# Kernel tuning notes

Measured on AMD Instinct MI355X. Metric: run time of the kernel, lower is better.

## Reference

```python
import jax, jax.numpy as jnp
import numpy as np

ALPHA = 0.2  # LeakyReLU negative slope
NEG_INF = jnp.float32(-9e15)


def setup_inputs() -> dict:
    key = jax.random.key(0)
    k1, k2, k3, k4, k5, k6 = jax.random.split(key, 6)
    B, N, F_in, F_out = 8, 2048, 256, 64
    h = jax.random.normal(k1, (B, N, F_in), dtype=jnp.float32)
    adj = jax.random.randint(k2, (B, N, N), 0, 2, dtype=jnp.int32)
    level = jax.random.uniform(k3, (B, N), dtype=jnp.float32)
    node_type = jax.random.uniform(k4, (B, N, N), dtype=jnp.float32)
    W = jax.random.normal(k5, (F_in, F_out), dtype=jnp.float32) * 1.414 / np.sqrt(F_in)
    a = jax.random.normal(k6, (2 * F_out, 1), dtype=jnp.float32) * 1.414 / np.sqrt(2 * F_out)
    return {"h": h, "adj": adj, "level": level, "node_type": node_type, "W": W, "a": a}


def reference(h, adj, level, node_type, W, a):
    # h: [B,N,Fin], adj/node_type: [B,N,N], level: [B,N], W: [Fin,Fout], a: [2*Fout,1]
    F_out = W.shape[1]
    Wh = jnp.einsum('bnf,fo->bno', h, W)  # [B,N,Fout]
    # Additive attention decomposed: e[b,i,j] = a1.Wh_i + a2.Wh_j (no O(N^2*2F) tensor)
    a1 = a[:F_out, 0]
    a2 = a[F_out:, 0]
    f1 = Wh @ a1  # [B,N]
    f2 = Wh @ a2  # [B,N]
    e = jax.nn.leaky_relu(f1[:, :, None] + f2[:, None, :], negative_slope=ALPHA)  # [B,N,N]
    # gat_our=True path: node_type scales scores, level scales Wh
    e = e * node_type
    Wh = Wh * level[:, :, None]
    attention = jnp.where(adj > 0, e, NEG_INF)
    attention = jax.nn.softmax(attention, axis=1)  # faithful: original softmax over dim=1
    # dropout p=0 / eval mode -> identity
    h_prime = jnp.einsum('bij,bjo->bio', attention, Wh)  # [B,N,Fout]
    return jax.nn.relu(h_prime)  # concat=True
```

## Files before the change

kernel.cpp:

```cpp
#include <hip/hip_runtime.h>

#define BB 8
#define NN 2048
#define FIN 256
#define FO 64

typedef short short8_t __attribute__((ext_vector_type(8)));
typedef float float4_t __attribute__((ext_vector_type(4)));

__device__ __forceinline__ unsigned short f2bf(float x) {
  unsigned int u = __float_as_uint(x);
  unsigned int r = (u + 0x7fffu + ((u >> 16) & 1u)) >> 16;
  return (unsigned short)r;
}

#define GLD16(gp, lp)                                                          \
  __builtin_amdgcn_global_load_lds(                                            \
      (const __attribute__((address_space(1))) void*)(gp),                     \
      (__attribute__((address_space(3))) void*)(lp), 16, 0, 0)

__global__ __launch_bounds__(256) void k1_gemm(
    const float* __restrict__ h,
    const float* __restrict__ level,
    const float* __restrict__ W,
    const float* __restrict__ a,
    float* __restrict__ V, float* __restrict__ f1, float* __restrict__ f2,
    float* __restrict__ scol)
{
  __shared__ float wlds[128 * 64];
  __shared__ float hs[16 * 260];
  __shared__ float parts1[16 * 17];
  __shared__ float parts2[16 * 17];
  int t = threadIdx.x;
  int b = blockIdx.x >> 7;
  int i0 = (blockIdx.x & 127) * 16;

  if (blockIdx.x < 64) scol[blockIdx.x * 256 + t] = 0.0f;

  {
    int r_ld = t >> 4, f0 = (t & 15) * 16;
    const float* hp = h + (size_t)(b * NN + i0 + r_ld) * FIN + f0;
    float4 x0 = *(const float4*)(hp);
    float4 x1 = *(const float4*)(hp + 4);
    float4 x2 = *(const float4*)(hp + 8);
    float4 x3 = *(const float4*)(hp + 12);
    float* hd = &hs[r_ld * 260 + f0];
    *(float4*)(hd + 0) = x0; *(float4*)(hd + 4) = x1;
    *(float4*)(hd + 8) = x2; *(float4*)(hd + 12) = x3;
  }

  int r = t >> 4;
  int c4 = (t & 15) * 4;
  float4 acc = {0, 0, 0, 0};

  #pragma unroll
  for (int half = 0; half < 2; ++half) {
    __syncthreads();
    #pragma unroll
    for (int q = 0; q < 8; ++q) {
      int idx = q * 1024 + t * 4;
      *(float4*)&wlds[idx] = *(const float4*)&W[half * 8192 + idx];
    }
    __syncthreads();
    for (int f = 0; f < 128; f += 8) {
      float4 hv0 = *(const float4*)&hs[r * 260 + half * 128 + f];
      float4 hv1 = *(const float4*)&hs[r * 260 + half * 128 + f + 4];
      float hvv[8] = {hv0.x, hv0.y, hv0.z, hv0.w, hv1.x, hv1.y, hv1.z, hv1.w};
      #pragma unroll
      for (int k = 0; k < 8; ++k) {
        float4 wv = *(const float4*)&wlds[(f + k) * 64 + c4];
        acc.x += hvv[k] * wv.x; acc.y += hvv[k] * wv.y;
        acc.z += hvv[k] * wv.z; acc.w += hvv[k] * wv.w;
      }
    }
  }

  float p1 = acc.x * a[c4] + acc.y * a[c4 + 1] + acc.z * a[c4 + 2] + acc.w * a[c4 + 3];
  float p2 = acc.x * a[64 + c4] + acc.y * a[64 + c4 + 1] +
             acc.z * a[64 + c4 + 2] + acc.w * a[64 + c4 + 3];
  parts1[r * 17 + (t & 15)] = p1;
  parts2[r * 17 + (t & 15)] = p2;
  __syncthreads();
  if (t < 16) {
    float s1 = 0.f, s2 = 0.f;
    #pragma unroll
    for (int g = 0; g < 16; ++g) { s1 += parts1[t * 17 + g]; s2 += parts2[t * 17 + g]; }
    f1[b * NN + i0 + t] = s1;
    f2[b * NN + i0 + t] = s2;
  }

  float lv = level[b * NN + i0 + r];
  float4 vv = {acc.x * lv, acc.y * lv, acc.z * lv, acc.w * lv};
  *(float4*)&V[(size_t)(b * NN + i0 + r) * FO + c4] = vv;
}

template <int STORE_U>
__global__ __launch_bounds__(512) void k2a_stats(
    const int* __restrict__ adj,
    const float* __restrict__ ntp,
    const float* __restrict__ f1,
    const float* __restrict__ f2,
    unsigned short* __restrict__ u_bf,
    unsigned char* __restrict__ bits,
    float* __restrict__ scol)
{
  __shared__ int ladj[2][16 * 256];
  __shared__ float lnt[2][16 * 256];
  __shared__ float red[2048];
  int t = threadIdx.x;
  int b = blockIdx.x >> 6;
  int row0 = (blockIdx.x & 63) * 32;
  int w = t >> 6, l = t & 63;
  size_t base = (size_t)b * NN;

  auto stage = [&](int buf, int s) {
    int tile = s >> 3, c = s & 7;
    int r0 = row0 + tile * 16 + 2 * w;
    const int* ga = adj + (base + r0) * NN + c * 256 + l * 4;
    const float* gn = ntp + (base + r0) * NN + c * 256 + l * 4;
    GLD16(ga, &ladj[buf][(2 * w) * 256]);
    GLD16(ga + NN, &ladj[buf][(2 * w + 1) * 256]);
    GLD16(gn, &lnt[buf][(2 * w) * 256]);
    GLD16(gn + NN, &lnt[buf][(2 * w + 1) * 256]);
  };

  int jj = t & 255;
  int rh = t >> 8;
  int kk_in = jj >> 5;
  int quad = (jj & 31) >> 3;
  int e = jj & 7;

  float accJ[8];
  #pragma unroll
  for (int c = 0; c < 8; ++c) accJ[c] = 0.f;
  float f2v[8];
  #pragma unroll
  for (int c = 0; c < 8; ++c) f2v[c] = f2[base + c * 256 + jj];

  stage(0, 0);
  for (int s = 0; s < 16; ++s) {
    int buf = s & 1;
    __syncthreads();
    if (s < 15) stage(buf ^ 1, s + 1);
    int tile = s >> 3, c = s & 7;
    int it = (row0 >> 4) + tile;
    size_t fbase = ((size_t)(b * 128 + it) * 64 + (c * 8 + kk_in)) * 512
                   + quad * 128 + rh * 64 + e;
    #pragma unroll
    for (int q = 0; q < 8; ++q) {
      int r = rh * 8 + q;
      int av = ladj[buf][r * 256 + jj];
      float nv = lnt[buf][r * 256 + jj];
      float f1v = f1[base + row0 + tile * 16 + r];
      float x = f1v + f2v[c];
      x = fmaxf(x, 0.2f * x);
      bool m = av > 0;
      float u = m ? __expf(x * nv) : 0.0f;
      accJ[c] += u;
      if (STORE_U) {
        u_bf[fbase + q * 8] = f2bf(u);
      } else {
        unsigned long long bal = __ballot(m);
        if (l == 0)
          *(unsigned long long*)&bits[(base + row0 + tile * 16 + r) * (NN / 8)
                                      + c * 32 + (w & 3) * 8] = bal;
      }
    }
  }

  if (rh == 0) {
    #pragma unroll
    for (int c = 0; c < 8; ++c) red[c * 256 + jj] = accJ[c];
  }
  __syncthreads();
  if (rh == 1) {
    #pragma unroll
    for (int c = 0; c < 8; ++c) red[c * 256 + jj] += accJ[c];
  }
  __syncthreads();
  #pragma unroll
  for (int q = 0; q < 4; ++q)
    atomicAdd(&scol[base + q * 512 + t], red[q * 512 + t]);
}

__global__ __launch_bounds__(256) void k2b_pack(
    const float* __restrict__ V,
    const float* __restrict__ scol,
    unsigned short* __restrict__ vf)
{
  int t = threadIdx.x;
  int b = blockIdx.x >> 6;
  int kk = blockIdx.x & 63;
  int ng = t >> 6;
  int l = t & 63;
  int jb = kk * 32 + ((l >> 4) * 8);
  int o = ng * 16 + (l & 15);
  unsigned int pk[4];
  #pragma unroll
  for (int p = 0; p < 4; ++p) {
    int jr0 = jb + 2 * p, jr1 = jb + 2 * p + 1;
    float s0 = scol[b * NN + jr0];
    float s1 = scol[b * NN + jr1];
    float i0 = (s0 > 0.f) ? (1.0f / s0) : 0.0f;
    float i1 = (s1 > 0.f) ? (1.0f / s1) : 0.0f;
    float v0 = V[(size_t)(b * NN + jr0) * FO + o] * i0;
    float v1 = V[(size_t)(b * NN + jr1) * FO + o] * i1;
    pk[p] = (unsigned int)f2bf(v0) | ((unsigned int)f2bf(v1) << 16);
  }
  *(uint4*)(vf + (size_t)(((b * 64 + kk) * 4 + ng) * 64 + l) * 8) =
      make_uint4(pk[0], pk[1], pk[2], pk[3]);
}

__global__ __launch_bounds__(256) void k3_agg_u(
    const unsigned short* __restrict__ u_bf,
    const unsigned short* __restrict__ vf,
    float* __restrict__ outp)
{
  __shared__ float red[4 * 16 * 68];
  int t = threadIdx.x;
  int b = blockIdx.x >> 7;
  int it = blockIdx.x & 127;
  int i0 = it * 16;
  int w = t >> 6, l = t & 63;
  int col = l & 15, quad = l >> 4;
  const unsigned short* abase = u_bf + ((size_t)(b * 128 + it) * 64) * 512 + l * 8;
  const unsigned short* vbase = vf + (size_t)(b * 64) * 2048 + l * 8;

  short8_t Aall[16];
  #pragma unroll
  for (int s = 0; s < 16; ++s)
    Aall[s] = *(const short8_t*)(abase + (size_t)(w * 16 + s) * 512);

  const unsigned short* vb0 = vbase + (size_t)(w * 16) * 2048;
  short8_t c0 = *(const short8_t*)(vb0);
  short8_t c1 = *(const short8_t*)(vb0 + 512);
  short8_t c2 = *(const short8_t*)(vb0 + 1024);
  short8_t c3 = *(const short8_t*)(vb0 + 1536);

  float4_t acc0 = {0, 0, 0, 0}, acc1 = {0, 0, 0, 0}, acc2 = {0, 0, 0, 0}, acc3 = {0, 0, 0, 0};

  #pragma unroll
  for (int s = 0; s < 16; ++s) {
    short8_t n0, n1, n2, n3;
    if (s < 15) {
      const unsigned short* vn = vbase + (size_t)(w * 16 + s + 1) * 2048;
      n0 = *(const short8_t*)(vn);
      n1 = *(const short8_t*)(vn + 512);
      n2 = *(const short8_t*)(vn + 1024);
      n3 = *(const short8_t*)(vn + 1536);
    }
    acc0 = __builtin_amdgcn_mfma_f32_16x16x32_bf16(Aall[s], c0, acc0, 0, 0, 0);
    acc1 = __builtin_amdgcn_mfma_f32_16x16x32_bf16(Aall[s], c1, acc1, 0, 0, 0);
    acc2 = __builtin_amdgcn_mfma_f32_16x16x32_bf16(Aall[s], c2, acc2, 0, 0, 0);
    acc3 = __builtin_amdgcn_mfma_f32_16x16x32_bf16(Aall[s], c3, acc3, 0, 0, 0);
    if (s < 15) { c0 = n0; c1 = n1; c2 = n2; c3 = n3; }
  }

  #pragma unroll
  for (int r = 0; r < 4; ++r) {
    int rowi = quad * 4 + r;
    red[w * 1088 + rowi * 68 + 0 + col] = acc0[r];
    red[w * 1088 + rowi * 68 + 16 + col] = acc1[r];
    red[w * 1088 + rowi * 68 + 32 + col] = acc2[r];
    red[w * 1088 + rowi * 68 + 48 + col] = acc3[r];
  }
  __syncthreads();

  int row = t >> 4, o4 = (t & 15) * 4;
  const float* rp = &red[row * 68 + o4];
  float4 s0 = *(const float4*)(rp);
  float4 s1 = *(const float4*)(rp + 1088);
  float4 s2 = *(const float4*)(rp + 2176);
  float4 s3 = *(const float4*)(rp + 3264);
  float4 o;
  o.x = fmaxf(s0.x + s1.x + s2.x + s3.x, 0.0f);
  o.y = fmaxf(s0.y + s1.y + s2.y + s3.y, 0.0f);
  o.z = fmaxf(s0.z + s1.z + s2.z + s3.z, 0.0f);
  o.w = fmaxf(s0.w + s1.w + s2.w + s3.w, 0.0f);
  *(float4*)&outp[(size_t)(b * NN + i0 + row) * FO + o4] = o;
}

__global__ __launch_bounds__(256) void k3_agg_b(
    const float* __restrict__ ntp,
    const unsigned char* __restrict__ bits,
    const float* __restrict__ f1,
    const float* __restrict__ f2,
    const unsigned short* __restrict__ vf,
    float* __restrict__ outp)
{
  __shared__ float red[4 * 16 * 68];
  int t = threadIdx.x;
  int b = blockIdx.x >> 7;
  int i0 = (blockIdx.x & 127) * 16;
  int w = t >> 6, l = t & 63;
  int col = l & 15, quad = l >> 4;
  int gi = b * NN + i0 + col;
  float f1v = f1[gi];
  const float* ntrow = ntp + (size_t)gi * NN;
  const unsigned char* brow = bits + (size_t)gi * (NN / 8);
  float4_t acc0 = {0, 0, 0, 0}, acc1 = {0, 0, 0, 0}, acc2 = {0, 0, 0, 0}, acc3 = {0, 0, 0, 0};

  for (int s = 0; s < 16; ++s) {
    int kk = w * 16 + s;
    int jq = kk * 32 + quad * 8;
    unsigned int m8 = brow[jq >> 3];
    float4 n0 = *(const float4*)(ntrow + jq);
    float4 n1 = *(const float4*)(ntrow + jq + 4);
    float4 g0 = *(const float4*)(f2 + b * NN + jq);
    float4 g1 = *(const float4*)(f2 + b * NN + jq + 4);
    float f2v[8] = {g0.x, g0.y, g0.z, g0.w, g1.x, g1.y, g1.z, g1.w};
    float ntf[8] = {n0.x, n0.y, n0.z, n0.w, n1.x, n1.y, n1.z, n1.w};
    union { unsigned int u[4]; short8_t v; } A;
    #pragma unroll
    for (int p = 0; p < 4; ++p) {
      int e0 = 2 * p, e1 = 2 * p + 1;
      float x0 = f1v + f2v[e0]; x0 = fmaxf(x0, 0.2f * x0);
      float u0 = ((m8 >> e0) & 1u) ? __expf(x0 * ntf[e0]) : 0.0f;
      float x1 = f1v + f2v[e1]; x1 = fmaxf(x1, 0.2f * x1);
      float u1 = ((m8 >> e1) & 1u) ? __expf(x1 * ntf[e1]) : 0.0f;
      A.u[p] = (unsigned int)f2bf(u0) | ((unsigned int)f2bf(u1) << 16);
    }
    const unsigned short* vb = vf + (size_t)(b * 64 + kk) * 2048 + l * 8;
    short8_t bf0 = *(const short8_t*)(vb);
    short8_t bf1 = *(const short8_t*)(vb + 512);
    short8_t bf2 = *(const short8_t*)(vb + 1024);
    short8_t bf3 = *(const short8_t*)(vb + 1536);
    acc0 = __builtin_amdgcn_mfma_f32_16x16x32_bf16(A.v, bf0, acc0, 0, 0, 0);
    acc1 = __builtin_amdgcn_mfma_f32_16x16x32_bf16(A.v, bf1, acc1, 0, 0, 0);
    acc2 = __builtin_amdgcn_mfma_f32_16x16x32_bf16(A.v, bf2, acc2, 0, 0, 0);
    acc3 = __builtin_amdgcn_mfma_f32_16x16x32_bf16(A.v, bf3, acc3, 0, 0, 0);
  }

  #pragma unroll
  for (int r = 0; r < 4; ++r) {
    int rowi = quad * 4 + r;
    red[w * 1088 + rowi * 68 + 0 + col] = acc0[r];
    red[w * 1088 + rowi * 68 + 16 + col] = acc1[r];
    red[w * 1088 + rowi * 68 + 32 + col] = acc2[r];
    red[w * 1088 + rowi * 68 + 48 + col] = acc3[r];
  }
  __syncthreads();

  int row = t >> 4, o4 = (t & 15) * 4;
  const float* rp = &red[row * 68 + o4];
  float4 s0 = *(const float4*)(rp);
  float4 s1 = *(const float4*)(rp + 1088);
  float4 s2 = *(const float4*)(rp + 2176);
  float4 s3 = *(const float4*)(rp + 3264);
  float4 o;
  o.x = fmaxf(s0.x + s1.x + s2.x + s3.x, 0.0f);
  o.y = fmaxf(s0.y + s1.y + s2.y + s3.y, 0.0f);
  o.z = fmaxf(s0.z + s1.z + s2.z + s3.z, 0.0f);
  o.w = fmaxf(s0.w + s1.w + s2.w + s3.w, 0.0f);
  *(float4*)&outp[(size_t)(b * NN + i0 + row) * FO + o4] = o;
}

extern "C" void kernel_launch(void* const* d_in, const int* in_sizes, int n_in,
                              void* d_out, int out_size, void* d_ws, size_t ws_size,
                              hipStream_t stream) {
  const float* h = (const float*)d_in[0];
  const int* adj = (const int*)d_in[1];
  const float* level = (const float*)d_in[2];
  const float* ntm = (const float*)d_in[3];
  const float* W = (const float*)d_in[4];
  const float* a = (const float*)d_in[5];
  float* outp = (float*)d_out;

  float* V = (float*)d_ws;
  float* f1 = V + (size_t)BB * NN * FO;
  float* f2 = f1 + BB * NN;
  float* scol = f2 + BB * NN;
  unsigned short* vf = (unsigned short*)(scol + BB * NN);
  char* tail = (char*)(vf + (size_t)BB * NN * FO);
  size_t fixed = (size_t)(tail - (char*)d_ws);
  size_t need_u = fixed + (size_t)BB * NN * NN * 2;
  bool big = (ws_size >= need_u);

  k1_gemm<<<1024, 256, 0, stream>>>(h, level, W, a, V, f1, f2, scol);
  if (big) {
    unsigned short* u_bf = (unsigned short*)tail;
    k2a_stats<1><<<512, 512, 0, stream>>>(adj, ntm, f1, f2, u_bf, nullptr, scol);
    k2b_pack<<<512, 256, 0, stream>>>(V, scol, vf);
    k3_agg_u<<<1024, 256, 0, stream>>>(u_bf, vf, outp);
  } else {
    unsigned char* bits = (unsigned char*)tail;
    k2a_stats<0><<<512, 512, 0, stream>>>(adj, ntm, f1, f2, nullptr, bits, scol);
    k2b_pack<<<512, 256, 0, stream>>>(V, scol, vf);
    k3_agg_b<<<1024, 256, 0, stream>>>(ntm, bits, f1, f2, vf, outp);
  }
}
```

Before: 346.6 us.

## Retile aggregation kernel to 64-row blocks with 8-wave K split

```diff
diff --git a/kernel.cpp b/kernel.cpp
--- a/kernel.cpp
+++ b/kernel.cpp
@@ -211,73 +211,88 @@
       make_uint4(pk[0], pk[1], pk[2], pk[3]);
 }
 
-__global__ __launch_bounds__(256) void k3_agg_u(
+__global__ __launch_bounds__(512) void k3_agg_u2(
     const unsigned short* __restrict__ u_bf,
     const unsigned short* __restrict__ vf,
     float* __restrict__ outp)
 {
-  __shared__ float red[4 * 16 * 68];
+  __shared__ float red[8 * 16 * 68];
   int t = threadIdx.x;
-  int b = blockIdx.x >> 7;
-  int it = blockIdx.x & 127;
-  int i0 = it * 16;
+  int b = blockIdx.x >> 5;
+  int tt = blockIdx.x & 31;
   int w = t >> 6, l = t & 63;
   int col = l & 15, quad = l >> 4;
-  const unsigned short* abase = u_bf + ((size_t)(b * 128 + it) * 64) * 512 + l * 8;
   const unsigned short* vbase = vf + (size_t)(b * 64) * 2048 + l * 8;
-
-  short8_t Aall[16];
-  #pragma unroll
-  for (int s = 0; s < 16; ++s)
-    Aall[s] = *(const short8_t*)(abase + (size_t)(w * 16 + s) * 512);
-
-  const unsigned short* vb0 = vbase + (size_t)(w * 16) * 2048;
-  short8_t c0 = *(const short8_t*)(vb0);
-  short8_t c1 = *(const short8_t*)(vb0 + 512);
-  short8_t c2 = *(const short8_t*)(vb0 + 1024);
-  short8_t c3 = *(const short8_t*)(vb0 + 1536);
-
-  float4_t acc0 = {0, 0, 0, 0}, acc1 = {0, 0, 0, 0}, acc2 = {0, 0, 0, 0}, acc3 = {0, 0, 0, 0};
-
-  #pragma unroll
-  for (int s = 0; s < 16; ++s) {
-    short8_t n0, n1, n2, n3;
-    if (s < 15) {
-      const unsigned short* vn = vbase + (size_t)(w * 16 + s + 1) * 2048;
-      n0 = *(const short8_t*)(vn);
-      n1 = *(const short8_t*)(vn + 512);
-      n2 = *(const short8_t*)(vn + 1024);
-      n3 = *(const short8_t*)(vn + 1536);
-    }
-    acc0 = __builtin_amdgcn_mfma_f32_16x16x32_bf16(Aall[s], c0, acc0, 0, 0, 0);
-    acc1 = __builtin_amdgcn_mfma_f32_16x16x32_bf16(Aall[s], c1, acc1, 0, 0, 0);
-    acc2 = __builtin_amdgcn_mfma_f32_16x16x32_bf16(Aall[s], c2, acc2, 0, 0, 0);
-    acc3 = __builtin_amdgcn_mfma_f32_16x16x32_bf16(Aall[s], c3, acc3, 0, 0, 0);
-    if (s < 15) { c0 = n0; c1 = n1; c2 = n2; c3 = n3; }
-  }
-
-  #pragma unroll
-  for (int r = 0; r < 4; ++r) {
-    int rowi = quad * 4 + r;
-    red[w * 1088 + rowi * 68 + 0 + col] = acc0[r];
-    red[w * 1088 + rowi * 68 + 16 + col] = acc1[r];
-    red[w * 1088 + rowi * 68 + 32 + col] = acc2[r];
-    red[w * 1088 + rowi * 68 + 48 + col] = acc3[r];
-  }
-  __syncthreads();
-
-  int row = t >> 4, o4 = (t & 15) * 4;
-  const float* rp = &red[row * 68 + o4];
-  float4 s0 = *(const float4*)(rp);
-  float4 s1 = *(const float4*)(rp + 1088);
-  float4 s2 = *(const float4*)(rp + 2176);
-  float4 s3 = *(const float4*)(rp + 3264);
-  float4 o;
-  o.x = fmaxf(s0.x + s1.x + s2.x + s3.x, 0.0f);
-  o.y = fmaxf(s0.y + s1.y + s2.y + s3.y, 0.0f);
-  o.z = fmaxf(s0.z + s1.z + s2.z + s3.z, 0.0f);
-  o.w = fmaxf(s0.w + s1.w + s2.w + s3.w, 0.0f);
-  *(float4*)&outp[(size_t)(b * NN + i0 + row) * FO + o4] = o;
+  const unsigned short* abase =
+      u_bf + ((size_t)(b * 128 + tt * 4) * 64) * 512 + l * 8;
+
+  float4_t acc[4][4];
+  #pragma unroll
+  for (int s = 0; s < 4; ++s)
+    #pragma unroll
+    for (int g = 0; g < 4; ++g) acc[s][g] = (float4_t){0, 0, 0, 0};
+
+  for (int s = 0; s < 8; ++s) {
+    int kk = w * 8 + s;
+    const unsigned short* vb = vbase + (size_t)kk * 2048;
+    short8_t c0 = *(const short8_t*)(vb);
+    short8_t c1 = *(const short8_t*)(vb + 512);
+    short8_t c2 = *(const short8_t*)(vb + 1024);
+    short8_t c3 = *(const short8_t*)(vb + 1536);
+    const unsigned short* ab = abase + (size_t)kk * 512;
+    short8_t A0 = *(const short8_t*)(ab);
+    short8_t A1 = *(const short8_t*)(ab + 64 * 512);
+    short8_t A2 = *(const short8_t*)(ab + 128 * 512);
+    short8_t A3 = *(const short8_t*)(ab + 192 * 512);
+    acc[0][0] = __builtin_amdgcn_mfma_f32_16x16x32_bf16(A0, c0, acc[0][0], 0, 0, 0);
+    acc[0][1] = __builtin_amdgcn_mfma_f32_16x16x32_bf16(A0, c1, acc[0][1], 0, 0, 0);
+    acc[0][2] = __builtin_amdgcn_mfma_f32_16x16x32_bf16(A0, c2, acc[0][2], 0, 0, 0);
+    acc[0][3] = __builtin_amdgcn_mfma_f32_16x16x32_bf16(A0, c3, acc[0][3], 0, 0, 0);
+    acc[1][0] = __builtin_amdgcn_mfma_f32_16x16x32_bf16(A1, c0, acc[1][0], 0, 0, 0);
+    acc[1][1] = __builtin_amdgcn_mfma_f32_16x16x32_bf16(A1, c1, acc[1][1], 0, 0, 0);
+    acc[1][2] = __builtin_amdgcn_mfma_f32_16x16x32_bf16(A1, c2, acc[1][2], 0, 0, 0);
+    acc[1][3] = __builtin_amdgcn_mfma_f32_16x16x32_bf16(A1, c3, acc[1][3], 0, 0, 0);
+    acc[2][0] = __builtin_amdgcn_mfma_f32_16x16x32_bf16(A2, c0, acc[2][0], 0, 0, 0);
+    acc[2][1] = __builtin_amdgcn_mfma_f32_16x16x32_bf16(A2, c1, acc[2][1], 0, 0, 0);
+    acc[2][2] = __builtin_amdgcn_mfma_f32_16x16x32_bf16(A2, c2, acc[2][2], 0, 0, 0);
+    acc[2][3] = __builtin_amdgcn_mfma_f32_16x16x32_bf16(A2, c3, acc[2][3], 0, 0, 0);
+    acc[3][0] = __builtin_amdgcn_mfma_f32_16x16x32_bf16(A3, c0, acc[3][0], 0, 0, 0);
+    acc[3][1] = __builtin_amdgcn_mfma_f32_16x16x32_bf16(A3, c1, acc[3][1], 0, 0, 0);
+    acc[3][2] = __builtin_amdgcn_mfma_f32_16x16x32_bf16(A3, c2, acc[3][2], 0, 0, 0);
+    acc[3][3] = __builtin_amdgcn_mfma_f32_16x16x32_bf16(A3, c3, acc[3][3], 0, 0, 0);
+  }
+
+  for (int sub = 0; sub < 4; ++sub) {
+    __syncthreads();
+    #pragma unroll
+    for (int r = 0; r < 4; ++r) {
+      int rowi = quad * 4 + r;
+      float* rp = &red[w * 1088 + rowi * 68 + col];
+      rp[0] = acc[sub][0][r];
+      rp[16] = acc[sub][1][r];
+      rp[32] = acc[sub][2][r];
+      rp[48] = acc[sub][3][r];
+    }
+    __syncthreads();
+    if (t < 256) {
+      int row = t >> 4, o4 = (t & 15) * 4;
+      const float* rp = &red[row * 68 + o4];
+      float4 s0 = *(const float4*)(rp);
+      float4 s1 = *(const float4*)(rp + 1088);
+      float4 s2 = *(const float4*)(rp + 2176);
+      float4 s3 = *(const float4*)(rp + 3264);
+      float4 s4 = *(const float4*)(rp + 4352);
+      float4 s5 = *(const float4*)(rp + 5440);
+      float4 s6 = *(const float4*)(rp + 6528);
+      float4 s7 = *(const float4*)(rp + 7616);
+      float4 o;
+      o.x = fmaxf(s0.x + s1.x + s2.x + s3.x + s4.x + s5.x + s6.x + s7.x, 0.0f);
+      o.y = fmaxf(s0.y + s1.y + s2.y + s3.y + s4.y + s5.y + s6.y + s7.y, 0.0f);
+      o.z = fmaxf(s0.z + s1.z + s2.z + s3.z + s4.z + s5.z + s6.z + s7.z, 0.0f);
+      o.w = fmaxf(s0.w + s1.w + s2.w + s3.w + s4.w + s5.w + s6.w + s7.w, 0.0f);
+      *(float4*)&outp[(size_t)(b * NN + tt * 64 + sub * 16 + row) * FO + o4] = o;
+    }
+  }
 }
 
 __global__ __launch_bounds__(256) void k3_agg_b(
@@ -381,7 +396,7 @@
     unsigned short* u_bf = (unsigned short*)tail;
     k2a_stats<1><<<512, 512, 0, stream>>>(adj, ntm, f1, f2, u_bf, nullptr, scol);
     k2b_pack<<<512, 256, 0, stream>>>(V, scol, vf);
-    k3_agg_u<<<1024, 256, 0, stream>>>(u_bf, vf, outp);
+    k3_agg_u2<<<256, 512, 0, stream>>>(u_bf, vf, outp);
   } else {
     unsigned char* bits = (unsigned char*)tail;
     k2a_stats<0><<<512, 512, 0, stream>>>(adj, ntm, f1, f2, nullptr, bits, scol);
```

Result: no change. 341.1 us (-1.6%).

## Store unnormalized attention row-major and stage it through LDS in aggregation

Applied to the files above, without the earlier changes.

```diff
diff --git a/kernel.cpp b/kernel.cpp
--- a/kernel.cpp
+++ b/kernel.cpp
@@ -18,6 +18,10 @@
   __builtin_amdgcn_global_load_lds(                                            \
       (const __attribute__((address_space(1))) void*)(gp),                     \
       (__attribute__((address_space(3))) void*)(lp), 16, 0, 0)
+#define GLD4(gp, lp)                                                           \
+  __builtin_amdgcn_global_load_lds(                                            \
+      (const __attribute__((address_space(1))) void*)(gp),                     \
+      (__attribute__((address_space(3))) void*)(lp), 4, 0, 0)
 
 __global__ __launch_bounds__(256) void k1_gemm(
     const float* __restrict__ h,
@@ -126,9 +130,6 @@
 
   int jj = t & 255;
   int rh = t >> 8;
-  int kk_in = jj >> 5;
-  int quad = (jj & 31) >> 3;
-  int e = jj & 7;
 
   float accJ[8];
   #pragma unroll
@@ -143,9 +144,6 @@
     __syncthreads();
     if (s < 15) stage(buf ^ 1, s + 1);
     int tile = s >> 3, c = s & 7;
-    int it = (row0 >> 4) + tile;
-    size_t fbase = ((size_t)(b * 128 + it) * 64 + (c * 8 + kk_in)) * 512
-                   + quad * 128 + rh * 64 + e;
     #pragma unroll
     for (int q = 0; q < 8; ++q) {
       int r = rh * 8 + q;
@@ -158,7 +156,7 @@
       float u = m ? __expf(x * nv) : 0.0f;
       accJ[c] += u;
       if (STORE_U) {
-        u_bf[fbase + q * 8] = f2bf(u);
+        u_bf[(base + row0 + tile * 16 + r) * NN + c * 256 + jj] = f2bf(u);
       } else {
         unsigned long long bal = __ballot(m);
         if (l == 0)
@@ -211,58 +209,64 @@
       make_uint4(pk[0], pk[1], pk[2], pk[3]);
 }
 
-__global__ __launch_bounds__(256) void k3_agg_u(
+__global__ __launch_bounds__(256) void k3_agg_u5(
     const unsigned short* __restrict__ u_bf,
     const unsigned short* __restrict__ vf,
     float* __restrict__ outp)
 {
-  __shared__ float red[4 * 16 * 68];
+  __shared__ __align__(16) unsigned short ub[2][16 * 264];
+  __shared__ float red[4 * 1088];
   int t = threadIdx.x;
   int b = blockIdx.x >> 7;
-  int it = blockIdx.x & 127;
-  int i0 = it * 16;
+  int tile = blockIdx.x & 127;
+  int i0 = tile * 16;
   int w = t >> 6, l = t & 63;
   int col = l & 15, quad = l >> 4;
-  const unsigned short* abase = u_bf + ((size_t)(b * 128 + it) * 64) * 512 + l * 8;
-  const unsigned short* vbase = vf + (size_t)(b * 64) * 2048 + l * 8;
-
-  short8_t Aall[16];
-  #pragma unroll
-  for (int s = 0; s < 16; ++s)
-    Aall[s] = *(const short8_t*)(abase + (size_t)(w * 16 + s) * 512);
-
-  const unsigned short* vb0 = vbase + (size_t)(w * 16) * 2048;
-  short8_t c0 = *(const short8_t*)(vb0);
-  short8_t c1 = *(const short8_t*)(vb0 + 512);
-  short8_t c2 = *(const short8_t*)(vb0 + 1024);
-  short8_t c3 = *(const short8_t*)(vb0 + 1536);
-
-  float4_t acc0 = {0, 0, 0, 0}, acc1 = {0, 0, 0, 0}, acc2 = {0, 0, 0, 0}, acc3 = {0, 0, 0, 0};
-
-  #pragma unroll
-  for (int s = 0; s < 16; ++s) {
-    short8_t n0, n1, n2, n3;
-    if (s < 15) {
-      const unsigned short* vn = vbase + (size_t)(w * 16 + s + 1) * 2048;
-      n0 = *(const short8_t*)(vn);
-      n1 = *(const short8_t*)(vn + 512);
-      n2 = *(const short8_t*)(vn + 1024);
-      n3 = *(const short8_t*)(vn + 1536);
-    }
-    acc0 = __builtin_amdgcn_mfma_f32_16x16x32_bf16(Aall[s], c0, acc0, 0, 0, 0);
-    acc1 = __builtin_amdgcn_mfma_f32_16x16x32_bf16(Aall[s], c1, acc1, 0, 0, 0);
-    acc2 = __builtin_amdgcn_mfma_f32_16x16x32_bf16(Aall[s], c2, acc2, 0, 0, 0);
-    acc3 = __builtin_amdgcn_mfma_f32_16x16x32_bf16(Aall[s], c3, acc3, 0, 0, 0);
-    if (s < 15) { c0 = n0; c1 = n1; c2 = n2; c3 = n3; }
+  size_t ubase = (size_t)(b * NN + i0) * NN;
+
+  auto stage = [&](int buf, int c) {
+    #pragma unroll
+    for (int r4 = 0; r4 < 4; ++r4) {
+      int r = w * 4 + r4;
+      const unsigned short* g = u_bf + ubase + (size_t)r * NN + c * 256 + l * 2;
+      GLD4(g, &ub[buf][r * 264]);
+      GLD4(g + 128, &ub[buf][r * 264 + 128]);
+    }
+  };
+
+  float4_t acc[4];
+  #pragma unroll
+  for (int g = 0; g < 4; ++g) acc[g] = (float4_t){0, 0, 0, 0};
+
+  stage(0, 0);
+  for (int c = 0; c < 8; ++c) {
+    int buf = c & 1;
+    __syncthreads();
+    if (c < 7) stage(buf ^ 1, c + 1);
+    #pragma unroll
+    for (int s = 0; s < 2; ++s) {
+      int kl = w * 2 + s;
+      int kk = c * 8 + kl;
+      short8_t A = *(const short8_t*)&ub[buf][col * 264 + kl * 32 + quad * 8];
+      const unsigned short* vb = vf + (size_t)(b * 64 + kk) * 2048 + l * 8;
+      short8_t c0 = *(const short8_t*)(vb);
+      short8_t c1 = *(const short8_t*)(vb + 512);
+      short8_t c2 = *(const short8_t*)(vb + 1024);
+      short8_t c3 = *(const short8_t*)(vb + 1536);
+      acc[0] = __builtin_amdgcn_mfma_f32_16x16x32_bf16(A, c0, acc[0], 0, 0, 0);
+      acc[1] = __builtin_amdgcn_mfma_f32_16x16x32_bf16(A, c1, acc[1], 0, 0, 0);
+      acc[2] = __builtin_amdgcn_mfma_f32_16x16x32_bf16(A, c2, acc[2], 0, 0, 0);
+      acc[3] = __builtin_amdgcn_mfma_f32_16x16x32_bf16(A, c3, acc[3], 0, 0, 0);
+    }
   }
 
   #pragma unroll
   for (int r = 0; r < 4; ++r) {
-    int rowi = quad * 4 + r;
-    red[w * 1088 + rowi * 68 + 0 + col] = acc0[r];
-    red[w * 1088 + rowi * 68 + 16 + col] = acc1[r];
-    red[w * 1088 + rowi * 68 + 32 + col] = acc2[r];
-    red[w * 1088 + rowi * 68 + 48 + col] = acc3[r];
+    float* rp = &red[w * 1088 + (quad * 4 + r) * 68 + col];
+    rp[0] = acc[0][r];
+    rp[16] = acc[1][r];
+    rp[32] = acc[2][r];
+    rp[48] = acc[3][r];
   }
   __syncthreads();
 
@@ -381,7 +385,7 @@
     unsigned short* u_bf = (unsigned short*)tail;
     k2a_stats<1><<<512, 512, 0, stream>>>(adj, ntm, f1, f2, u_bf, nullptr, scol);
     k2b_pack<<<512, 256, 0, stream>>>(V, scol, vf);
-    k3_agg_u<<<1024, 256, 0, stream>>>(u_bf, vf, outp);
+    k3_agg_u5<<<1024, 256, 0, stream>>>(u_bf, vf, outp);
   } else {
     unsigned char* bits = (unsigned char*)tail;
     k2a_stats<0><<<512, 512, 0, stream>>>(adj, ntm, f1, f2, nullptr, bits, scol);
```

Result: faster. 337.8 us (-2.5%).
